# Kernel tuning notes

Measured on AMD Instinct MI355X. Metric: run time of the kernel, lower is better.

Reference implementation:

```python
import jax, jax.numpy as jnp
import numpy as np

B, N, D = 4, 64, 64          # batch, n_nodes, state_dim
FN, FE, INTER, T = 32, 16, 128, 3


def setup_inputs() -> dict:
    key = jax.random.key(0)
    ks = jax.random.split(key, 12)
    conn = (jax.random.uniform(ks[0], (B, N * N, 1)) < 0.3).astype(jnp.float32)
    feat = jax.random.uniform(ks[1], (B, N * N, FE - 1))
    edges = jnp.concatenate([conn, feat], axis=-1)
    nodes = jax.random.normal(ks[2], (B, N, FN))
    adjacency = jnp.zeros((B, N * N, 1))  # unused (adjacency=False)
    s = lambda i, sh, fan: jax.random.normal(ks[i], sh) * (1.0 / np.sqrt(fan))
    return dict(
        edges=edges, nodes=nodes, adjacency=adjacency,
        W_en=s(3, (FN, D), FN), b_en=jnp.zeros(D),
        W_agg=s(4, (FE, D * D), FE), b_agg=jnp.zeros(D * D),
        W_ih=s(5, (3 * D, D), D), W_hh=s(6, (3 * D, D), D),
        b_ih=jnp.zeros(3 * D), b_hh=jnp.zeros(3 * D),
        W_r1=s(7, (2 * D + FE, INTER), 2 * D + FE), b_r1=jnp.zeros(INTER),
        W_r2=s(8, (INTER, INTER), INTER), b_r2=jnp.zeros(INTER),
        W_r3=s(9, (INTER, 1), INTER), b_r3=jnp.zeros(1),
    )


def _gru_cell(x, h, W_ih, W_hh, b_ih, b_hh):
    # PyTorch nn.GRU cell: gates ordered (r, z, n)
    gi = x @ W_ih.T + b_ih
    gh = h @ W_hh.T + b_hh
    ir, iz, inn = jnp.split(gi, 3, axis=-1)
    hr, hz, hn = jnp.split(gh, 3, axis=-1)
    r = jax.nn.sigmoid(ir + hr)
    z = jax.nn.sigmoid(iz + hz)
    n = jnp.tanh(inn + r * hn)
    return (1.0 - z) * n + z * h


def reference(edges, nodes, adjacency, W_en, b_en, W_agg, b_agg,
              W_ih, W_hh, b_ih, b_hh, W_r1, b_r1, W_r2, b_r2, W_r3, b_r3):
    # mask: torch.where(x==0, x, ones) on first edge feature -> {0,1}
    mask = jnp.where(edges[..., :1] == 0, 0.0, 1.0)  # [B, N*N, 1]
    h = jax.nn.relu(nodes @ W_en + b_en)  # [B, N, D]
    for _ in range(T):
        # per-edge dynamic weight matrices A: [B, N*N, D, D]
        A = jax.nn.relu(edges @ W_agg + b_agg).reshape(B, N * N, D, D)
        node_j = jnp.tile(h, (1, N, 1))  # [B, N*N, D]
        msgs = jnp.einsum('beij,bej->bei', A, node_j) * mask  # [B, N*N, D]
        agg = msgs.reshape(B, N, N, D).sum(2)  # [B, N, D]
        hf = h.reshape(-1, D)
        af = agg.reshape(-1, D)
        # GRU over length-2 sequence [old_state, agg_messages], h0 = 0; take last
        h1 = _gru_cell(hf, jnp.zeros_like(hf), W_ih, W_hh, b_ih, b_hh)
        h2 = _gru_cell(af, h1, W_ih, W_hh, b_ih, b_hh)
        h = h2.reshape(B, N, D)
    # Readout over all node pairs
    state_i = jnp.repeat(h, N, axis=1)      # [B, N*N, D] (node i repeated)
    state_j = jnp.tile(h, (1, N, 1))        # [B, N*N, D]
    cat = jnp.concatenate([state_i, edges, state_j], axis=-1)
    a1 = jax.nn.relu(cat @ W_r1 + b_r1)
    a2 = jax.nn.relu(a1 @ W_r2 + b_r2)
    return a2 @ W_r3 + b_r3  # [B, N*N, 1]
```

## Files before the change

kernel.cpp:

```cpp
#include <hip/hip_runtime.h>

typedef float float4v __attribute__((ext_vector_type(4)));

__device__ __forceinline__ float sigm(float x) { return 1.0f / (1.0f + __expf(-x)); }

#define HS_LD 68

__global__ __launch_bounds__(1024) void k_it(
    const float* __restrict__ edges, const float* __restrict__ nodes,
    const float* __restrict__ W_en, const float* __restrict__ b_en,
    const float* __restrict__ W_agg, const float* __restrict__ b_agg,
    const float* __restrict__ W_ih, const float* __restrict__ W_hh,
    const float* __restrict__ b_ih, const float* __restrict__ b_hh,
    const float* __restrict__ h_cur, float* __restrict__ h_next,
    const float* __restrict__ W_r1, const float* __restrict__ b_r1,
    float* __restrict__ Ha, float* __restrict__ Hc, int it0, int emit)
{
    __shared__ float hs[64 * HS_LD];
    __shared__ float eL[64 * 16];
    __shared__ int   jn[64];
    __shared__ int   nES;
    __shared__ float xtra[768];

    int t = threadIdx.x;
    int row = blockIdx.x;
    int ri = row & 63;
    int b = row >> 6;

    if (it0) {
#pragma unroll
        for (int q = 0; q < 4; ++q) {
            int idx = q * 1024 + t;
            int n = idx >> 6, d = idx & 63;
            const float* np_ = nodes + ((b << 6) + n) * 32;
            float acc = b_en[d];
#pragma unroll
            for (int k = 0; k < 32; ++k)
                acc = fmaf(np_[k], W_en[k * 64 + d], acc);
            hs[n * HS_LD + d] = fmaxf(acc, 0.f);
        }
    } else {
        int n = t >> 4, col = (t & 15) * 4;
        *(float4v*)(hs + n * HS_LD + col) =
            *(const float4v*)(h_cur + ((b << 6) + n) * 64 + col);
    }

    if (t < 64) {
        const float* ep = edges + ((size_t)row * 64 + t) * 16;
        float f0 = ep[0];
        unsigned long long m = __ballot(f0 != 0.f);
        if (t == 0) nES = __popcll(m);
        if (f0 != 0.f) {
            int pos = __popcll(m & ((1ull << t) - 1ull));
            jn[pos] = t;
            float* dst = eL + pos * 16;
#pragma unroll
            for (int u = 0; u < 4; ++u)
                *(float4v*)(dst + u * 4) = *(const float4v*)(ep + u * 4);
        }
    }

    int dim = t >> 4, c4 = t & 15;
    float4v w[16];
    {
        const float* wp = W_agg + dim * 64 + c4 * 4;
#pragma unroll
        for (int k = 0; k < 16; ++k)
            w[k] = *(const float4v*)(wp + k * 4096);
    }
    float4v bias = *(const float4v*)(b_agg + dim * 64 + c4 * 4);

    __syncthreads();
    int nE = nES;

    float rsum = 0.f;
    for (int s = 0; s < nE; ++s) {
        const float* eP = eL + s * 16;
        float4v e0 = *(const float4v*)(eP);
        float4v e1 = *(const float4v*)(eP + 4);
        float4v e2 = *(const float4v*)(eP + 8);
        float4v e3 = *(const float4v*)(eP + 12);
        int ej = jn[s];
        float4v a = bias;
#pragma unroll
        for (int k = 0; k < 4; ++k) {
#pragma unroll
            for (int u = 0; u < 4; ++u) a[u] = fmaf(e0[k], w[k][u], a[u]);
        }
#pragma unroll
        for (int k = 0; k < 4; ++k) {
#pragma unroll
            for (int u = 0; u < 4; ++u) a[u] = fmaf(e1[k], w[4 + k][u], a[u]);
        }
#pragma unroll
        for (int k = 0; k < 4; ++k) {
#pragma unroll
            for (int u = 0; u < 4; ++u) a[u] = fmaf(e2[k], w[8 + k][u], a[u]);
        }
#pragma unroll
        for (int k = 0; k < 4; ++k) {
#pragma unroll
            for (int u = 0; u < 4; ++u) a[u] = fmaf(e3[k], w[12 + k][u], a[u]);
        }
        float4v hv = *(const float4v*)(hs + ej * HS_LD + c4 * 4);
#pragma unroll
        for (int u = 0; u < 4; ++u)
            rsum = fmaf(fmaxf(a[u], 0.f), hv[u], rsum);
    }
#pragma unroll
    for (int m = 1; m < 16; m <<= 1) rsum += __shfl_xor(rsum, m, 64);
    float* aggS = xtra;
    if (c4 == 0) aggS[dim] = rsum;
    __syncthreads();

    float* g1  = xtra + 64;
    float* h1S = xtra + 256;
    float* g2i = xtra + 320;
    float* g2h = xtra + 512;
    float* hnS = xtra + 704;
    const float* hrow = hs + ri * HS_LD;

    if (t < 192) {
        float g = b_ih[t];
        const float* wr = W_ih + t * 64;
#pragma unroll
        for (int k = 0; k < 64; ++k) g = fmaf(hrow[k], wr[k], g);
        g1[t] = g;
    }
    __syncthreads();
    if (t < 64) {
        float r1 = sigm(g1[t] + b_hh[t]);
        float z1 = sigm(g1[64 + t] + b_hh[64 + t]);
        float nn1 = tanhf(g1[128 + t] + r1 * b_hh[128 + t]);
        h1S[t] = (1.f - z1) * nn1;
    }
    __syncthreads();
    if (t < 192) {
        float gi = b_ih[t];
        float gh = b_hh[t];
        const float* wri = W_ih + t * 64;
        const float* wrh = W_hh + t * 64;
#pragma unroll
        for (int k = 0; k < 64; ++k) {
            gi = fmaf(aggS[k], wri[k], gi);
            gh = fmaf(h1S[k], wrh[k], gh);
        }
        g2i[t] = gi; g2h[t] = gh;
    }
    __syncthreads();
    if (t < 64) {
        float r = sigm(g2i[t] + g2h[t]);
        float z = sigm(g2i[64 + t] + g2h[64 + t]);
        float nn = tanhf(g2i[128 + t] + r * g2h[128 + t]);
        float hn = (1.f - z) * nn + z * h1S[t];
        h_next[row * 64 + t] = hn;
        hnS[t] = hn;
    }
    __syncthreads();
    if (emit && t < 256) {
        int m = t >> 7, d = t & 127;
        const float* wbase = W_r1 + (m ? 80 * 128 : 0) + d;
        float acc = m ? 0.f : b_r1[d];
#pragma unroll
        for (int k = 0; k < 64; ++k)
            acc = fmaf(hnS[k], wbase[k * 128], acc);
        if (m == 0) Ha[row * 128 + d] = acc;
        else        Hc[row * 128 + d] = acc;
    }
}

__global__ __launch_bounds__(256) void k_read(
    const float* __restrict__ edges,
    const float* __restrict__ Ha, const float* __restrict__ Hc,
    const float* __restrict__ W_r1,
    const float* __restrict__ W_r2, const float* __restrict__ b_r2,
    const float* __restrict__ W_r3, const float* __restrict__ b_r3,
    float* __restrict__ out)
{
    __shared__ float HaS[128];
    __shared__ float eS[32 * 16];
    __shared__ float A1[32 * 128];
    int t = threadIdx.x;
    int unit = blockIdx.x;
    int row = unit >> 1, qp = unit & 1;
    int b = row >> 6;

    const float* src = Hc + (size_t)((b << 6) + qp * 32) * 128;
#pragma unroll
    for (int r = 0; r < 4; ++r) {
        int off = (r * 256 + t) * 4;
        *(float4v*)(A1 + off) = *(const float4v*)(src + off);
    }
    if (t < 32)
        *(float4v*)(HaS + t * 4) = *(const float4v*)(Ha + (size_t)row * 128 + t * 4);
    if (t < 128)
        *(float4v*)(eS + t * 4) =
            *(const float4v*)(edges + ((size_t)row * 64 + qp * 32) * 16 + t * 4);
    __syncthreads();

    int td = t & 31, pg = t >> 5;

    float4v ew0 = {0,0,0,0}, ew1 = ew0, ew2 = ew0, ew3 = ew0;
#pragma unroll
    for (int k = 0; k < 16; ++k) {
        float4v wk = *(const float4v*)(W_r1 + (64 + k) * 128 + td * 4);
        float e0 = eS[(pg * 4 + 0) * 16 + k];
        float e1 = eS[(pg * 4 + 1) * 16 + k];
        float e2 = eS[(pg * 4 + 2) * 16 + k];
        float e3 = eS[(pg * 4 + 3) * 16 + k];
#pragma unroll
        for (int u = 0; u < 4; ++u) {
            ew0[u] = fmaf(e0, wk[u], ew0[u]);
            ew1[u] = fmaf(e1, wk[u], ew1[u]);
            ew2[u] = fmaf(e2, wk[u], ew2[u]);
            ew3[u] = fmaf(e3, wk[u], ew3[u]);
        }
    }
    float4v ha = *(const float4v*)(HaS + td * 4);
#pragma unroll
    for (int pi = 0; pi < 4; ++pi) {
        float4v ew = (pi == 0) ? ew0 : (pi == 1) ? ew1 : (pi == 2) ? ew2 : ew3;
        float* slot = A1 + (pg * 4 + pi) * 128 + td * 4;
        float4v hc = *(const float4v*)slot;
        float4v a;
#pragma unroll
        for (int u = 0; u < 4; ++u) a[u] = fmaxf(hc[u] + ha[u] + ew[u], 0.f);
        *(float4v*)slot = a;
    }
    __syncthreads();

    float4v bb2 = *(const float4v*)(b_r2 + td * 4);
    float4v acc0 = bb2, acc1 = bb2, acc2 = bb2, acc3 = bb2;
    for (int k4 = 0; k4 < 32; ++k4) {
        float4v wA = *(const float4v*)(W_r2 + (k4 * 4 + 0) * 128 + td * 4);
        float4v wB = *(const float4v*)(W_r2 + (k4 * 4 + 1) * 128 + td * 4);
        float4v wC = *(const float4v*)(W_r2 + (k4 * 4 + 2) * 128 + td * 4);
        float4v wD = *(const float4v*)(W_r2 + (k4 * 4 + 3) * 128 + td * 4);
        float4v a0 = *(const float4v*)(A1 + (pg * 4 + 0) * 128 + k4 * 4);
        float4v a1 = *(const float4v*)(A1 + (pg * 4 + 1) * 128 + k4 * 4);
        float4v a2 = *(const float4v*)(A1 + (pg * 4 + 2) * 128 + k4 * 4);
        float4v a3 = *(const float4v*)(A1 + (pg * 4 + 3) * 128 + k4 * 4);
#pragma unroll
        for (int u = 0; u < 4; ++u) {
            acc0[u] = fmaf(a0[0], wA[u], acc0[u]);
            acc0[u] = fmaf(a0[1], wB[u], acc0[u]);
            acc0[u] = fmaf(a0[2], wC[u], acc0[u]);
            acc0[u] = fmaf(a0[3], wD[u], acc0[u]);
            acc1[u] = fmaf(a1[0], wA[u], acc1[u]);
            acc1[u] = fmaf(a1[1], wB[u], acc1[u]);
            acc1[u] = fmaf(a1[2], wC[u], acc1[u]);
            acc1[u] = fmaf(a1[3], wD[u], acc1[u]);
            acc2[u] = fmaf(a2[0], wA[u], acc2[u]);
            acc2[u] = fmaf(a2[1], wB[u], acc2[u]);
            acc2[u] = fmaf(a2[2], wC[u], acc2[u]);
            acc2[u] = fmaf(a2[3], wD[u], acc2[u]);
            acc3[u] = fmaf(a3[0], wA[u], acc3[u]);
            acc3[u] = fmaf(a3[1], wB[u], acc3[u]);
            acc3[u] = fmaf(a3[2], wC[u], acc3[u]);
            acc3[u] = fmaf(a3[3], wD[u], acc3[u]);
        }
    }

    float4v w3v = *(const float4v*)(W_r3 + td * 4);
    float b3 = b_r3[0];
    float p0 = fmaxf(acc0[0], 0.f) * w3v[0] + fmaxf(acc0[1], 0.f) * w3v[1]
             + fmaxf(acc0[2], 0.f) * w3v[2] + fmaxf(acc0[3], 0.f) * w3v[3];
    float p1 = fmaxf(acc1[0], 0.f) * w3v[0] + fmaxf(acc1[1], 0.f) * w3v[1]
             + fmaxf(acc1[2], 0.f) * w3v[2] + fmaxf(acc1[3], 0.f) * w3v[3];
    float p2 = fmaxf(acc2[0], 0.f) * w3v[0] + fmaxf(acc2[1], 0.f) * w3v[1]
             + fmaxf(acc2[2], 0.f) * w3v[2] + fmaxf(acc2[3], 0.f) * w3v[3];
    float p3 = fmaxf(acc3[0], 0.f) * w3v[0] + fmaxf(acc3[1], 0.f) * w3v[1]
             + fmaxf(acc3[2], 0.f) * w3v[2] + fmaxf(acc3[3], 0.f) * w3v[3];
#pragma unroll
    for (int m = 1; m < 32; m <<= 1) {
        p0 += __shfl_xor(p0, m, 64);
        p1 += __shfl_xor(p1, m, 64);
        p2 += __shfl_xor(p2, m, 64);
        p3 += __shfl_xor(p3, m, 64);
    }
    if (td == 0) {
        int obase = row * 64 + qp * 32 + pg * 4;
        out[obase + 0] = p0 + b3;
        out[obase + 1] = p1 + b3;
        out[obase + 2] = p2 + b3;
        out[obase + 3] = p3 + b3;
    }
}

extern "C" void kernel_launch(void* const* d_in, const int* in_sizes, int n_in,
                              void* d_out, int out_size, void* d_ws, size_t ws_size,
                              hipStream_t stream)
{
    const float* edges = (const float*)d_in[0];
    const float* nodes = (const float*)d_in[1];
    const float* W_en  = (const float*)d_in[3];
    const float* b_en  = (const float*)d_in[4];
    const float* W_agg = (const float*)d_in[5];
    const float* b_agg = (const float*)d_in[6];
    const float* W_ih  = (const float*)d_in[7];
    const float* W_hh  = (const float*)d_in[8];
    const float* b_ih  = (const float*)d_in[9];
    const float* b_hh  = (const float*)d_in[10];
    const float* W_r1  = (const float*)d_in[11];
    const float* b_r1  = (const float*)d_in[12];
    const float* W_r2  = (const float*)d_in[13];
    const float* b_r2  = (const float*)d_in[14];
    const float* W_r3  = (const float*)d_in[15];
    const float* b_r3  = (const float*)d_in[16];

    float* hA = (float*)d_ws;
    float* hB = hA + 16384;
    float* Ha = hB + 16384;
    float* Hc = Ha + 256 * 128;
    float* out = (float*)d_out;

    k_it<<<256, 1024, 0, stream>>>(edges, nodes, W_en, b_en, W_agg, b_agg,
                                   W_ih, W_hh, b_ih, b_hh, hA, hA,
                                   W_r1, b_r1, Ha, Hc, 1, 0);
    k_it<<<256, 1024, 0, stream>>>(edges, nodes, W_en, b_en, W_agg, b_agg,
                                   W_ih, W_hh, b_ih, b_hh, hA, hB,
                                   W_r1, b_r1, Ha, Hc, 0, 0);
    k_it<<<256, 1024, 0, stream>>>(edges, nodes, W_en, b_en, W_agg, b_agg,
                                   W_ih, W_hh, b_ih, b_hh, hB, hA,
                                   W_r1, b_r1, Ha, Hc, 0, 1);
    k_read<<<512, 256, 0, stream>>>(edges, Ha, Hc, W_r1, W_r2, b_r2,
                                    W_r3, b_r3, out);
}
```

Before: 83.19 us.

## Halve k_it block size with 8-wide per-thread W_agg slices; hoist GRU gate matvec

k_it now runs 512 threads per block instead of 1024. Each thread keeps 32 float4 registers of W_agg covering 8 output columns instead of 4, which halves the shuffle-reduction width and doubles the FMA work per edge per thread. The first GRU input-gate matvec (g1) is moved ahead of the edge-message loop, so threads below 192 compute it before the loop and one barrier is dropped. The cost is higher register pressure (128 VGPRs for weights) and fewer threads to hide latency in the edge loop.

```diff
diff --git a/kernel.cpp b/kernel.cpp
--- a/kernel.cpp
+++ b/kernel.cpp
@@ -6,7 +6,7 @@
 
 #define HS_LD 68
 
-__global__ __launch_bounds__(1024) void k_it(
+__global__ __launch_bounds__(512) void k_it(
     const float* __restrict__ edges, const float* __restrict__ nodes,
     const float* __restrict__ W_en, const float* __restrict__ b_en,
     const float* __restrict__ W_agg, const float* __restrict__ b_agg,
@@ -29,8 +29,8 @@
 
     if (it0) {
 #pragma unroll
-        for (int q = 0; q < 4; ++q) {
-            int idx = q * 1024 + t;
+        for (int q = 0; q < 8; ++q) {
+            int idx = q * 512 + t;
             int n = idx >> 6, d = idx & 63;
             const float* np_ = nodes + ((b << 6) + n) * 32;
             float acc = b_en[d];
@@ -40,9 +40,11 @@
             hs[n * HS_LD + d] = fmaxf(acc, 0.f);
         }
     } else {
-        int n = t >> 4, col = (t & 15) * 4;
-        *(float4v*)(hs + n * HS_LD + col) =
-            *(const float4v*)(h_cur + ((b << 6) + n) * 64 + col);
+        int n = t >> 3, col = (t & 7) * 8;
+        const float* gp = h_cur + ((b << 6) + n) * 64 + col;
+        float* lp = hs + n * HS_LD + col;
+        *(float4v*)(lp)     = *(const float4v*)(gp);
+        *(float4v*)(lp + 4) = *(const float4v*)(gp + 4);
     }
 
     if (t < 64) {
@@ -60,18 +62,37 @@
         }
     }
 
-    int dim = t >> 4, c4 = t & 15;
-    float4v w[16];
+    int dim = t >> 3, c8 = t & 7;
+    float4v w[32];
     {
-        const float* wp = W_agg + dim * 64 + c4 * 4;
-#pragma unroll
-        for (int k = 0; k < 16; ++k)
-            w[k] = *(const float4v*)(wp + k * 4096);
-    }
-    float4v bias = *(const float4v*)(b_agg + dim * 64 + c4 * 4);
+        const float* wp = W_agg + dim * 64 + c8 * 8;
+#pragma unroll
+        for (int k = 0; k < 16; ++k) {
+            w[2 * k]     = *(const float4v*)(wp + k * 4096);
+            w[2 * k + 1] = *(const float4v*)(wp + k * 4096 + 4);
+        }
+    }
+    float4v bias0 = *(const float4v*)(b_agg + dim * 64 + c8 * 8);
+    float4v bias1 = *(const float4v*)(b_agg + dim * 64 + c8 * 8 + 4);
 
     __syncthreads();
     int nE = nES;
+
+    float* aggS = xtra;
+    float* g1  = xtra + 64;
+    float* h1S = xtra + 256;
+    float* g2i = xtra + 320;
+    float* g2h = xtra + 512;
+    float* hnS = xtra + 704;
+    const float* hrow = hs + ri * HS_LD;
+
+    if (t < 192) {
+        float g = b_ih[t];
+        const float* wr = W_ih + t * 64;
+#pragma unroll
+        for (int k = 0; k < 64; ++k) g = fmaf(hrow[k], wr[k], g);
+        g1[t] = g;
+    }
 
     float rsum = 0.f;
     for (int s = 0; s < nE; ++s) {
@@ -81,53 +102,54 @@
         float4v e2 = *(const float4v*)(eP + 8);
         float4v e3 = *(const float4v*)(eP + 12);
         int ej = jn[s];
-        float4v a = bias;
+        float4v a0 = bias0, a1 = bias1;
 #pragma unroll
         for (int k = 0; k < 4; ++k) {
 #pragma unroll
-            for (int u = 0; u < 4; ++u) a[u] = fmaf(e0[k], w[k][u], a[u]);
+            for (int u = 0; u < 4; ++u) {
+                a0[u] = fmaf(e0[k], w[2 * k][u], a0[u]);
+                a1[u] = fmaf(e0[k], w[2 * k + 1][u], a1[u]);
+            }
         }
 #pragma unroll
         for (int k = 0; k < 4; ++k) {
 #pragma unroll
-            for (int u = 0; u < 4; ++u) a[u] = fmaf(e1[k], w[4 + k][u], a[u]);
+            for (int u = 0; u < 4; ++u) {
+                a0[u] = fmaf(e1[k], w[2 * (4 + k)][u], a0[u]);
+                a1[u] = fmaf(e1[k], w[2 * (4 + k) + 1][u], a1[u]);
+            }
         }
 #pragma unroll
         for (int k = 0; k < 4; ++k) {
 #pragma unroll
-            for (int u = 0; u < 4; ++u) a[u] = fmaf(e2[k], w[8 + k][u], a[u]);
+            for (int u = 0; u < 4; ++u) {
+                a0[u] = fmaf(e2[k], w[2 * (8 + k)][u], a0[u]);
+                a1[u] = fmaf(e2[k], w[2 * (8 + k) + 1][u], a1[u]);
+            }
         }
 #pragma unroll
         for (int k = 0; k < 4; ++k) {
 #pragma unroll
-            for (int u = 0; u < 4; ++u) a[u] = fmaf(e3[k], w[12 + k][u], a[u]);
-        }
-        float4v hv = *(const float4v*)(hs + ej * HS_LD + c4 * 4);
-#pragma unroll
-        for (int u = 0; u < 4; ++u)
-            rsum = fmaf(fmaxf(a[u], 0.f), hv[u], rsum);
-    }
-#pragma unroll
-    for (int m = 1; m < 16; m <<= 1) rsum += __shfl_xor(rsum, m, 64);
-    float* aggS = xtra;
-    if (c4 == 0) aggS[dim] = rsum;
-    __syncthreads();
-
-    float* g1  = xtra + 64;
-    float* h1S = xtra + 256;
-    float* g2i = xtra + 320;
-    float* g2h = xtra + 512;
-    float* hnS = xtra + 704;
-    const float* hrow = hs + ri * HS_LD;
-
-    if (t < 192) {
-        float g = b_ih[t];
-        const float* wr = W_ih + t * 64;
-#pragma unroll
-        for (int k = 0; k < 64; ++k) g = fmaf(hrow[k], wr[k], g);
-        g1[t] = g;
-    }
-    __syncthreads();
+            for (int u = 0; u < 4; ++u) {
+                a0[u] = fmaf(e3[k], w[2 * (12 + k)][u], a0[u]);
+                a1[u] = fmaf(e3[k], w[2 * (12 + k) + 1][u], a1[u]);
+            }
+        }
+        const float* hp = hs + ej * HS_LD + c8 * 8;
+        float4v hv0 = *(const float4v*)(hp);
+        float4v hv1 = *(const float4v*)(hp + 4);
+#pragma unroll
+        for (int u = 0; u < 4; ++u) {
+            rsum = fmaf(fmaxf(a0[u], 0.f), hv0[u], rsum);
+            rsum = fmaf(fmaxf(a1[u], 0.f), hv1[u], rsum);
+        }
+    }
+
+#pragma unroll
+    for (int m = 1; m < 8; m <<= 1) rsum += __shfl_xor(rsum, m, 64);
+    if (c8 == 0) aggS[dim] = rsum;
+    __syncthreads();
+
     if (t < 64) {
         float r1 = sigm(g1[t] + b_hh[t]);
         float z1 = sigm(g1[64 + t] + b_hh[64 + t]);
@@ -314,15 +336,15 @@
     float* Hc = Ha + 256 * 128;
     float* out = (float*)d_out;
 
-    k_it<<<256, 1024, 0, stream>>>(edges, nodes, W_en, b_en, W_agg, b_agg,
-                                   W_ih, W_hh, b_ih, b_hh, hA, hA,
-                                   W_r1, b_r1, Ha, Hc, 1, 0);
-    k_it<<<256, 1024, 0, stream>>>(edges, nodes, W_en, b_en, W_agg, b_agg,
-                                   W_ih, W_hh, b_ih, b_hh, hA, hB,
-                                   W_r1, b_r1, Ha, Hc, 0, 0);
-    k_it<<<256, 1024, 0, stream>>>(edges, nodes, W_en, b_en, W_agg, b_agg,
-                                   W_ih, W_hh, b_ih, b_hh, hB, hA,
-                                   W_r1, b_r1, Ha, Hc, 0, 1);
+    k_it<<<256, 512, 0, stream>>>(edges, nodes, W_en, b_en, W_agg, b_agg,
+                                  W_ih, W_hh, b_ih, b_hh, hA, hA,
+                                  W_r1, b_r1, Ha, Hc, 1, 0);
+    k_it<<<256, 512, 0, stream>>>(edges, nodes, W_en, b_en, W_agg, b_agg,
+                                  W_ih, W_hh, b_ih, b_hh, hA, hB,
+                                  W_r1, b_r1, Ha, Hc, 0, 0);
+    k_it<<<256, 512, 0, stream>>>(edges, nodes, W_en, b_en, W_agg, b_agg,
+                                  W_ih, W_hh, b_ih, b_hh, hB, hA,
+                                  W_r1, b_r1, Ha, Hc, 0, 1);
     k_read<<<512, 256, 0, stream>>>(edges, Ha, Hc, W_r1, W_r2, b_r2,
                                     W_r3, b_r3, out);
 }
```

After: 78.53 us, median of 2. 1.06x faster.
